# Optimization experiments

Hardware: AMD Instinct MI355X
Metric: run time of the kernel (lower is better)

Reference implementation:

```python
import jax, jax.numpy as jnp
import numpy as np

S, D, H, HD = 3072, 1280, 16, 80
FF = 4 * D
EPS = 1e-6


def layernorm(x, scale, bias):
    mu = jnp.mean(x, axis=-1, keepdims=True)
    var = jnp.mean(jnp.square(x - mu), axis=-1, keepdims=True)
    return (x - mu) * jax.lax.rsqrt(var + EPS) * scale + bias


def rotate_half(x):
    x1 = x[..., : x.shape[-1] // 2]
    x2 = x[..., x.shape[-1] // 2 :]
    return jnp.concatenate([-x2, x1], axis=-1)


def apply_rope(x, freqs):
    # x: (S,H,hd), freqs: (S,hd/2)
    cos = jnp.repeat(jnp.cos(freqs), 2, axis=-1)[:, None, :]  # (S,1,hd)
    sin = jnp.repeat(jnp.sin(freqs), 2, axis=-1)[:, None, :]
    return x * cos + rotate_half(x) * sin


def quick_gelu(x):
    return x * jax.nn.sigmoid(1.702 * x)


def setup_inputs() -> dict:
    key = jax.random.key(0)
    ks = jax.random.split(key, 12)
    s = 0.02
    return {
        "hidden_states": jax.random.normal(ks[0], (S, D), jnp.float32),
        "rotary_pos_emb": jax.random.normal(ks[1], (S, HD // 2), jnp.float32),
        "ln1_scale": jnp.ones((D,), jnp.float32),
        "ln1_bias": jnp.zeros((D,), jnp.float32),
        "ln2_scale": jnp.ones((D,), jnp.float32),
        "ln2_bias": jnp.zeros((D,), jnp.float32),
        "qkv_w": jax.random.normal(ks[2], (D, 3 * D), jnp.float32) * s,
        "qkv_b": jnp.zeros((3 * D,), jnp.float32),
        "proj_w": jax.random.normal(ks[3], (D, D), jnp.float32) * s,
        "proj_b": jnp.zeros((D,), jnp.float32),
        "fc1_w": jax.random.normal(ks[4], (D, FF), jnp.float32) * s,
        "fc1_b": jnp.zeros((FF,), jnp.float32),
        "fc2_w": jax.random.normal(ks[5], (FF, D), jnp.float32) * s,
        "fc2_b": jnp.zeros((D,), jnp.float32),
        "cu_seqlens": jnp.array([0, 1024, 2048, 3072], jnp.int32),
    }


def reference(hidden_states, rotary_pos_emb, ln1_scale, ln1_bias, ln2_scale,
              ln2_bias, qkv_w, qkv_b, proj_w, proj_b, fc1_w, fc1_b, fc2_w,
              fc2_b, cu_seqlens):
    x = hidden_states  # (S, D)
    h = layernorm(x, ln1_scale, ln1_bias)
    qkv = (h @ qkv_w + qkv_b).reshape(S, 3, H, HD)
    q, k, v = qkv[:, 0], qkv[:, 1], qkv[:, 2]  # each (S, H, hd)
    q = apply_rope(q, rotary_pos_emb)
    k = apply_rope(k, rotary_pos_emb)

    # block-diagonal varlen mask from cu_seqlens (same segment attends)
    ids = jnp.arange(S)
    seg = jnp.searchsorted(cu_seqlens, ids, side="right")  # (S,)
    valid = seg[:, None] == seg[None, :]  # (S, S)
    bias = jnp.where(valid, 0.0, jnp.finfo(q.dtype).min)

    scale = 1.0 / jnp.sqrt(jnp.asarray(HD, q.dtype))
    scores = jnp.einsum("qhd,khd->hqk", q, k) * scale + bias
    probs = jax.nn.softmax(scores.astype(jnp.float32), axis=-1).astype(q.dtype)
    attn = jnp.einsum("hqk,khd->qhd", probs, v).reshape(S, D)
    attn = attn @ proj_w + proj_b

    x = x + attn
    h2 = layernorm(x, ln2_scale, ln2_bias)
    mlp = quick_gelu(h2 @ fc1_w + fc1_b) @ fc2_w + fc2_b
    return x + mlp
```

## Files before the change

kernel.cpp:

```cpp
#include <hip/hip_runtime.h>

typedef __bf16 bf16x8 __attribute__((ext_vector_type(8)));
typedef float f32x4 __attribute__((ext_vector_type(4)));
typedef unsigned short u16;
typedef u16 u16x4 __attribute__((ext_vector_type(4)));
typedef u16 u16x8 __attribute__((ext_vector_type(8)));
typedef float float4v __attribute__((ext_vector_type(4)));

__device__ __forceinline__ u16 f2bf(float f) {
    __bf16 b = (__bf16)f;
    return __builtin_bit_cast(unsigned short, b);
}
__device__ __forceinline__ float bf2f(u16 x) {
    __bf16 b = __builtin_bit_cast(__bf16, x);
    return (float)b;
}

__device__ __forceinline__ void gld16(const void* g, void* l) {
    __builtin_amdgcn_global_load_lds((const __attribute__((address_space(1))) void*)g,
                                     (__attribute__((address_space(3))) void*)l, 16, 0, 0);
}

__device__ __forceinline__ int xcd_swz(int orig, int nwg) {
    const int q = nwg >> 3, r = nwg & 7;
    const int xcd = orig & 7, pos = orig >> 3;
    return (xcd < r ? xcd * (q + 1) : r * (q + 1) + (xcd - r) * q) + pos;
}

__global__ __launch_bounds__(256) void transpose_kernel(
    const float* __restrict__ W, u16* __restrict__ WT, int K, int N)
{
    __shared__ u16 tile[64][65];
    const int tx = threadIdx.x & 63, ty = threadIdx.x >> 6;
    const int n0 = blockIdx.x * 64, k0 = blockIdx.y * 64;
    #pragma unroll
    for (int i = ty; i < 64; i += 4)
        tile[i][tx] = f2bf(W[(size_t)(k0 + i) * N + n0 + tx]);
    __syncthreads();
    #pragma unroll
    for (int i = ty; i < 64; i += 4)
        WT[(size_t)(n0 + i) * K + k0 + tx] = tile[tx][i];
}

__global__ __launch_bounds__(256) void ln_kernel(
    const float* __restrict__ x, const float* __restrict__ sc,
    const float* __restrict__ bias, u16* __restrict__ out)
{
    const int row = blockIdx.x, t = threadIdx.x;
    const float* xr = x + (size_t)row * 1280;
    float v[5], s1 = 0.f, s2 = 0.f;
    #pragma unroll
    for (int i = 0; i < 5; i++) {
        v[i] = xr[t + i * 256];
        s1 += v[i];
        s2 += v[i] * v[i];
    }
    #pragma unroll
    for (int off = 32; off; off >>= 1) {
        s1 += __shfl_down(s1, off);
        s2 += __shfl_down(s2, off);
    }
    __shared__ float rA[4], rB[4];
    if ((t & 63) == 0) { rA[t >> 6] = s1; rB[t >> 6] = s2; }
    __syncthreads();
    s1 = rA[0] + rA[1] + rA[2] + rA[3];
    s2 = rB[0] + rB[1] + rB[2] + rB[3];
    const float mu = s1 * (1.f / 1280.f);
    const float var = s2 * (1.f / 1280.f) - mu * mu;
    const float rstd = rsqrtf(var + 1e-6f);
    #pragma unroll
    for (int i = 0; i < 5; i++) {
        const int d = t + i * 256;
        out[(size_t)row * 1280 + d] = f2bf((v[i] - mu) * rstd * sc[d] + bias[d]);
    }
}

template <int GELU, int OUTB, int SPLIT>
__global__ __launch_bounds__(512, 2) void gemm256_kernel(
    const u16* __restrict__ A, const u16* __restrict__ BT,
    const float* __restrict__ bias,
    float* __restrict__ outF, u16* __restrict__ outB,
    int M, int N, int K)
{
    __shared__ u16 As[2][256 * 64];
    __shared__ u16 Bs[2][256 * 64];
    const int tid = threadIdx.x, lane = tid & 63, wave = tid >> 6;
    const int nwg = gridDim.x * gridDim.y;
    const int bid = xcd_swz(blockIdx.y * gridDim.x + blockIdx.x, nwg);
    const int m0 = (bid / gridDim.x) * 256, n0 = (bid % gridDim.x) * 256;
    const int wr = wave >> 2, wc = wave & 3;
    const int wm = wr * 128, wn = wc * 64;
    const int lr = lane & 15, lh = lane >> 4;

    const int kchunk = K / SPLIT;
    const int kz = (SPLIT > 1) ? blockIdx.z : 0;
    const int kbeg = kz * kchunk;
    const int niter = kchunk >> 7;

    const int sr = lane >> 3;
    const int sc8 = (lane & 7) ^ sr;

    f32x4 acc[8][4] = {};
    bf16x8 bq[4][2];

    auto stgA = [&](int t, int h) {
        const int buf = t & 1;
        #pragma unroll
        for (int j = 0; j < 2; j++) {
            const int row = h * 128 + j * 64 + wave * 8 + sr;
            gld16(A + (size_t)(m0 + row) * K + kbeg + t * 64 + sc8 * 8,
                  &As[buf][h * 8192 + j * 4096 + wave * 512]);
        }
    };
    auto stgB = [&](int t, int h) {
        const int buf = t & 1;
        #pragma unroll
        for (int j = 0; j < 2; j++) {
            const int row = h * 128 + j * 64 + wave * 8 + sr;
            gld16(BT + (size_t)(n0 + row) * K + kbeg + t * 64 + sc8 * 8,
                  &Bs[buf][h * 8192 + j * 4096 + wave * 512]);
        }
    };

#define PHASE(BUF, Q, STGSTMT, WAITSTMT)                                        \
    {                                                                           \
        if ((Q) == 0) {                                                         \
            _Pragma("unroll") for (int ni = 0; ni < 4; ni++) {                  \
                const int row = wn + ni * 16 + lr;                              \
                _Pragma("unroll") for (int kk = 0; kk < 2; kk++)                \
                    bq[ni][kk] = *reinterpret_cast<const bf16x8*>(              \
                        &Bs[BUF][row * 64 + ((kk * 4 + lh) ^ (row & 7)) * 8]);  \
            }                                                                   \
        }                                                                       \
        bf16x8 afq[2][2];                                                       \
        _Pragma("unroll") for (int m2 = 0; m2 < 2; m2++) {                      \
            const int row = wm + (Q) * 32 + m2 * 16 + lr;                       \
            _Pragma("unroll") for (int kk = 0; kk < 2; kk++)                    \
                afq[m2][kk] = *reinterpret_cast<const bf16x8*>(                 \
                    &As[BUF][row * 64 + ((kk * 4 + lh) ^ (row & 7)) * 8]);      \
        }                                                                       \
        STGSTMT;                                                                \
        __builtin_amdgcn_s_barrier();                                           \
        asm volatile("s_waitcnt lgkmcnt(0)" ::: "memory");                      \
        __builtin_amdgcn_s_setprio(1);                                          \
        _Pragma("unroll") for (int kk = 0; kk < 2; kk++)                        \
            _Pragma("unroll") for (int m2 = 0; m2 < 2; m2++)                    \
                _Pragma("unroll") for (int ni = 0; ni < 4; ni++)                \
                    acc[(Q) * 2 + m2][ni] =                                     \
                        __builtin_amdgcn_mfma_f32_16x16x32_bf16(                \
                            afq[m2][kk], bq[ni][kk], acc[(Q) * 2 + m2][ni],     \
                            0, 0, 0);                                           \
        __builtin_amdgcn_s_setprio(0);                                          \
        WAITSTMT;                                                               \
        __builtin_amdgcn_s_barrier();                                           \
    }

    stgB(0, 0); stgB(0, 1);
    stgA(0, 0); stgA(0, 1);
    stgB(1, 0); stgB(1, 1);
    asm volatile("s_waitcnt vmcnt(4)" ::: "memory");
    __builtin_amdgcn_s_barrier();

    for (int i = 0; i < niter - 1; i++) {
        const int t0 = 2 * i, t1 = 2 * i + 1;
        PHASE(0, 0, stgA(t1, 0), (void)0);
        PHASE(0, 1, stgA(t1, 1), (void)0);
        PHASE(0, 2, stgB(t0 + 2, 0), (void)0);
        PHASE(0, 3, stgB(t0 + 2, 1),
              asm volatile("s_waitcnt vmcnt(4)" ::: "memory"));
        PHASE(1, 0, stgA(t0 + 2, 0), (void)0);
        PHASE(1, 1, stgA(t0 + 2, 1), (void)0);
        PHASE(1, 2, stgB(t1 + 2, 0), (void)0);
        PHASE(1, 3, stgB(t1 + 2, 1),
              asm volatile("s_waitcnt vmcnt(4)" ::: "memory"));
    }
    {
        const int t1 = 2 * niter - 1;
        PHASE(0, 0, stgA(t1, 0), (void)0);
        PHASE(0, 1, stgA(t1, 1), (void)0);
        PHASE(0, 2, (void)0, (void)0);
        PHASE(0, 3, (void)0,
              asm volatile("s_waitcnt vmcnt(0)" ::: "memory"));
        PHASE(1, 0, (void)0, (void)0);
        PHASE(1, 1, (void)0, (void)0);
        PHASE(1, 2, (void)0, (void)0);
        PHASE(1, 3, (void)0, (void)0);
    }
#undef PHASE

    if (SPLIT > 1) {
        float* pf = outF + (size_t)kz * M * N;
        #pragma unroll
        for (int mi = 0; mi < 8; mi++)
            #pragma unroll
            for (int ni = 0; ni < 4; ni++) {
                const int col = n0 + wn + ni * 16 + lr;
                #pragma unroll
                for (int r = 0; r < 4; r++) {
                    const int rowg = m0 + wm + mi * 16 + lh * 4 + r;
                    pf[(size_t)rowg * N + col] = acc[mi][ni][r];
                }
            }
        return;
    }

    #pragma unroll
    for (int mi = 0; mi < 8; mi++) {
        #pragma unroll
        for (int ni = 0; ni < 4; ni++) {
            const int col = n0 + wn + ni * 16 + lr;
            const float bv = bias[col];
            #pragma unroll
            for (int r = 0; r < 4; r++) {
                const int rowg = m0 + wm + mi * 16 + lh * 4 + r;
                float v = acc[mi][ni][r] + bv;
                if (GELU) v = v * (1.0f / (1.0f + __expf(-1.702f * v)));
                if (OUTB) outB[(size_t)rowg * N + col] = f2bf(v);
            }
        }
    }
}

template <int GELU, int RES, int OUTF, int OUTB, int SPLIT>
__global__ __launch_bounds__(256) void gemm_kernel(
    const u16* __restrict__ A, const u16* __restrict__ BT,
    const float* __restrict__ bias, const float* __restrict__ res,
    float* __restrict__ outF, u16* __restrict__ outB,
    int M, int N, int K)
{
    __shared__ u16 As[128 * 64];
    __shared__ u16 Bs[128 * 64];
    const int tid = threadIdx.x, lane = tid & 63, wave = tid >> 6;
    const int nwg = gridDim.x * gridDim.y;
    const int bid = xcd_swz(blockIdx.y * gridDim.x + blockIdx.x, nwg);
    const int m0 = (bid / gridDim.x) * 128, n0 = (bid % gridDim.x) * 128;
    const int wm = (wave >> 1) * 64, wn = (wave & 1) * 64;
    const int lr = lane & 15, lh = lane >> 4;
    const int srow = lane >> 3;
    const int schunk = (lane & 7) ^ (srow & 7);

    const int kchunk = K / SPLIT;
    const int kz = (SPLIT > 1) ? blockIdx.z : 0;
    const int kbeg = kz * kchunk, kend = kbeg + kchunk;

    f32x4 acc[4][4] = {};

    for (int k0 = kbeg; k0 < kend; k0 += 64) {
        #pragma unroll
        for (int s = 0; s < 4; s++) {
            const int seg = wave + s * 4;
            const int row = seg * 8 + srow;
            gld16(A + (size_t)(m0 + row) * K + k0 + schunk * 8, &As[seg * 512]);
            gld16(BT + (size_t)(n0 + row) * K + k0 + schunk * 8, &Bs[seg * 512]);
        }
        asm volatile("s_waitcnt vmcnt(0)" ::: "memory");
        __syncthreads();

        bf16x8 af[4][2], bfr[4][2];
        #pragma unroll
        for (int mi = 0; mi < 4; mi++) {
            const int row = wm + mi * 16 + lr;
            #pragma unroll
            for (int kk = 0; kk < 2; kk++) {
                const int cb = (kk * 64 + lh * 16) ^ ((row & 7) << 4);
                af[mi][kk] = *reinterpret_cast<const bf16x8*>((const char*)As + row * 128 + cb);
            }
        }
        #pragma unroll
        for (int ni = 0; ni < 4; ni++) {
            const int row = wn + ni * 16 + lr;
            #pragma unroll
            for (int kk = 0; kk < 2; kk++) {
                const int cb = (kk * 64 + lh * 16) ^ ((row & 7) << 4);
                bfr[ni][kk] = *reinterpret_cast<const bf16x8*>((const char*)Bs + row * 128 + cb);
            }
        }
        #pragma unroll
        for (int kk = 0; kk < 2; kk++)
            #pragma unroll
            for (int mi = 0; mi < 4; mi++)
                #pragma unroll
                for (int ni = 0; ni < 4; ni++)
                    acc[mi][ni] = __builtin_amdgcn_mfma_f32_16x16x32_bf16(
                        af[mi][kk], bfr[ni][kk], acc[mi][ni], 0, 0, 0);
        __syncthreads();
    }

    if (SPLIT > 1) {
        float* pf = outF + (size_t)kz * M * N;
        #pragma unroll
        for (int mi = 0; mi < 4; mi++)
            #pragma unroll
            for (int ni = 0; ni < 4; ni++) {
                const int col = n0 + wn + ni * 16 + lr;
                #pragma unroll
                for (int r = 0; r < 4; r++) {
                    const int rowg = m0 + wm + mi * 16 + lh * 4 + r;
                    pf[(size_t)rowg * N + col] = acc[mi][ni][r];
                }
            }
        return;
    }

    #pragma unroll
    for (int mi = 0; mi < 4; mi++) {
        #pragma unroll
        for (int ni = 0; ni < 4; ni++) {
            const int col = n0 + wn + ni * 16 + lr;
            const float bv = bias[col];
            #pragma unroll
            for (int r = 0; r < 4; r++) {
                const int rowg = m0 + wm + mi * 16 + lh * 4 + r;
                float v = acc[mi][ni][r] + bv;
                if (RES) v += res[(size_t)rowg * N + col];
                if (GELU) v = v * (1.0f / (1.0f + __expf(-1.702f * v)));
                if (OUTF) outF[(size_t)rowg * N + col] = v;
                if (OUTB) outB[(size_t)rowg * N + col] = f2bf(v);
            }
        }
    }
}

__global__ __launch_bounds__(256) void reduce4_kernel(
    const float* __restrict__ parts, const float* __restrict__ bias,
    const float* __restrict__ res, float* __restrict__ out, int N, size_t MN)
{
    const size_t i4 = ((size_t)blockIdx.x * 256 + threadIdx.x) * 4;
    if (i4 >= MN) return;
    float4v a = *reinterpret_cast<const float4v*>(parts + i4);
    a += *reinterpret_cast<const float4v*>(parts + MN + i4);
    a += *reinterpret_cast<const float4v*>(parts + 2 * MN + i4);
    a += *reinterpret_cast<const float4v*>(parts + 3 * MN + i4);
    a += *reinterpret_cast<const float4v*>(res + i4);
    const int col = (int)(i4 % N);
    a += *reinterpret_cast<const float4v*>(bias + col);
    *reinterpret_cast<float4v*>(out + i4) = a;
}

__global__ __launch_bounds__(256) void rope_kernel(
    const u16* __restrict__ qkv, const float* __restrict__ freqs,
    u16* __restrict__ qp, u16* __restrict__ kp, u16* __restrict__ vt)
{
    const int s = blockIdx.x, t = threadIdx.x;
    const float scale = 0.1118033988749895f;
    __shared__ float cs[40], sn[40];
    if (t < 40) {
        const float f = freqs[(size_t)s * 40 + t];
        cs[t] = cosf(f);
        sn[t] = sinf(f);
    }
    __syncthreads();
    const u16* row = qkv + (size_t)s * 3840;
    for (int i = t; i < 1280; i += 256) {
        const int h = i / 80, d = i % 80;
        const float c = cs[d >> 1], sv = sn[d >> 1];
        const float q0 = bf2f(row[i]);
        const float q1 = (d < 40) ? -bf2f(row[i + 40]) : bf2f(row[i - 40]);
        qp[((size_t)h * 3072 + s) * 96 + d] = f2bf((q0 * c + q1 * sv) * scale);
        const float k0 = bf2f(row[1280 + i]);
        const float k1 = (d < 40) ? -bf2f(row[1280 + i + 40]) : bf2f(row[1280 + i - 40]);
        kp[((size_t)h * 3072 + s) * 128 + d] = f2bf(k0 * c + k1 * sv);
        vt[((size_t)h * 80 + d) * 3072 + s] = row[2560 + i];
    }
    {
        const int h = t / 16, d = 80 + (t % 16);
        qp[((size_t)h * 3072 + s) * 96 + d] = 0;
    }
    for (int i = t; i < 768; i += 256) {
        const int h = i / 48, d = 80 + (i % 48);
        kp[((size_t)h * 3072 + s) * 128 + d] = 0;
    }
}

__global__ __launch_bounds__(256) void attn_kernel(
    const u16* __restrict__ qp, const u16* __restrict__ kp,
    const u16* __restrict__ vt, u16* __restrict__ attn_out)
{
    const int tid = threadIdx.x, lane = tid & 63, wave = tid >> 6;
    const int w = xcd_swz(blockIdx.x, 768);
    const int qt = w & 15;
    const int h = (w >> 4) & 15;
    const int sq = w >> 8;
    const int lr = lane & 15, lh = lane >> 4;
    const int qrow = sq * 1024 + qt * 64 + wave * 16;

    __shared__ u16 Ks[2][64 * 128];
    __shared__ u16 Vs[2][80 * 64];
    __shared__ u16 P[4][16 * 72];

    bf16x8 aq[3];
    {
        const u16* qb = qp + ((size_t)h * 3072 + qrow + lr) * 96 + lh * 8;
        #pragma unroll
        for (int d0 = 0; d0 < 3; d0++)
            aq[d0] = *reinterpret_cast<const bf16x8*>(qb + d0 * 32);
    }

    float m = -1e30f, l = 0.f;
    f32x4 acc[5] = {};

    const u16* kseg = kp + ((size_t)h * 3072 + sq * 1024) * 128;
    const u16* vseg = vt + (size_t)h * 80 * 3072 + sq * 1024;

    const int krow_l = lane >> 4;
    const int kch    = lane & 15;
    const int vrow_l = lane >> 3;
    const int vch    = lane & 7;

    auto stageK = [&](int t, int buf) {
        #pragma unroll
        for (int s = 0; s < 4; s++) {
            const int seg = wave + s * 4;
            const int row = seg * 4 + krow_l;
            gld16(kseg + (size_t)(t * 64 + row) * 128 + ((kch ^ (row & 7)) * 8),
                  &Ks[buf][seg * 512]);
        }
    };
    auto stageV = [&](int t, int buf) {
        #pragma unroll
        for (int s = 0; s < 3; s++) {
            const int seg = wave + s * 4;
            if (seg < 10) {
                const int row = seg * 8 + vrow_l;
                gld16(vseg + (size_t)row * 3072 + t * 64 + ((vch ^ (row & 7)) * 8),
                      &Vs[buf][seg * 512]);
            }
        }
    };

    stageK(0, 0);
    stageV(0, 0);
    asm volatile("s_waitcnt vmcnt(0)" ::: "memory");
    __syncthreads();

    for (int t = 0; t < 16; t++) {
        const int cur = t & 1;
        if (t < 15) {
            stageK(t + 1, cur ^ 1);
            stageV(t + 1, cur ^ 1);
        }

        f32x4 sc[4] = {};
        #pragma unroll
        for (int c = 0; c < 4; c++) {
            #pragma unroll
            for (int d0 = 0; d0 < 3; d0++) {
                const int row = c * 16 + lr;
                const int rb = row * 256 + (((d0 * 4 + lh) ^ (row & 7)) << 4);
                bf16x8 kf = *reinterpret_cast<const bf16x8*>((const char*)Ks[cur] + rb);
                sc[c] = __builtin_amdgcn_mfma_f32_16x16x32_bf16(kf, aq[d0], sc[c], 0, 0, 0);
            }
        }

        float pmax = sc[0][0];
        #pragma unroll
        for (int c = 0; c < 4; c++)
            #pragma unroll
            for (int r = 0; r < 4; r++)
                pmax = fmaxf(pmax, sc[c][r]);
        pmax = fmaxf(pmax, __shfl_xor(pmax, 16));
        pmax = fmaxf(pmax, __shfl_xor(pmax, 32));

        if (!__all(pmax - m <= 8.0f)) {
            const float mn = fmaxf(m, pmax);
            const float fac = __expf(m - mn);
            m = mn;
            l *= fac;
            #pragma unroll
            for (int df = 0; df < 5; df++)
                #pragma unroll
                for (int r = 0; r < 4; r++)
                    acc[df][r] *= fac;
        }

        float p[4][4], rs = 0.f;
        #pragma unroll
        for (int c = 0; c < 4; c++)
            #pragma unroll
            for (int r = 0; r < 4; r++) {
                p[c][r] = __expf(sc[c][r] - m);
                rs += p[c][r];
            }
        rs += __shfl_xor(rs, 16);
        rs += __shfl_xor(rs, 32);
        l += rs;

        #pragma unroll
        for (int c = 0; c < 4; c++) {
            u16x4 pw;
            #pragma unroll
            for (int r = 0; r < 4; r++)
                pw[r] = f2bf(p[c][r]);
            *reinterpret_cast<u16x4*>((char*)P[wave] + lr * 144 + c * 32 + lh * 8) = pw;
        }
        asm volatile("s_waitcnt lgkmcnt(0)" ::: "memory");

        #pragma unroll
        for (int ks = 0; ks < 2; ks++) {
            bf16x8 pa = *reinterpret_cast<const bf16x8*>(
                (const char*)P[wave] + lr * 144 + ks * 64 + lh * 16);
            #pragma unroll
            for (int df = 0; df < 5; df++) {
                const int row = df * 16 + lr;
                const int vb = row * 128 + (((ks * 4 + lh) ^ (row & 7)) << 4);
                bf16x8 vf = *reinterpret_cast<const bf16x8*>((const char*)Vs[cur] + vb);
                acc[df] = __builtin_amdgcn_mfma_f32_16x16x32_bf16(vf, pa, acc[df], 0, 0, 0);
            }
        }

        asm volatile("s_waitcnt vmcnt(0)" ::: "memory");
        __syncthreads();
    }

    const float invl = 1.0f / l;
    u16* orow = attn_out + (size_t)(qrow + lr) * 1280 + h * 80;
    #pragma unroll
    for (int df = 0; df < 5; df++) {
        u16x4 o;
        #pragma unroll
        for (int r = 0; r < 4; r++)
            o[r] = f2bf(acc[df][r] * invl);
        *reinterpret_cast<u16x4*>(orow + df * 16 + lh * 4) = o;
    }
}

extern "C" void kernel_launch(void* const* d_in, const int* in_sizes, int n_in,
                              void* d_out, int out_size, void* d_ws, size_t ws_size,
                              hipStream_t stream) {
    const float* hidden = (const float*)d_in[0];
    const float* rot    = (const float*)d_in[1];
    const float* ln1s   = (const float*)d_in[2];
    const float* ln1b   = (const float*)d_in[3];
    const float* ln2s   = (const float*)d_in[4];
    const float* ln2b   = (const float*)d_in[5];
    const float* qkvw   = (const float*)d_in[6];
    const float* qkvb   = (const float*)d_in[7];
    const float* projw  = (const float*)d_in[8];
    const float* projb  = (const float*)d_in[9];
    const float* fc1w   = (const float*)d_in[10];
    const float* fc1b   = (const float*)d_in[11];
    const float* fc2w   = (const float*)d_in[12];
    const float* fc2b   = (const float*)d_in[13];
    float* out = (float*)d_out;

    char* p = (char*)d_ws;
    auto alloc = [&](size_t n) { char* r = p; p += (n + 255) & ~(size_t)255; return r; };
    u16* qkvwT  = (u16*)alloc((size_t)3840 * 1280 * 2);
    u16* projwT = (u16*)alloc((size_t)1280 * 1280 * 2);
    u16* fc1wT  = (u16*)alloc((size_t)5120 * 1280 * 2);
    u16* fc2wT  = (u16*)alloc((size_t)1280 * 5120 * 2);
    u16* hbuf   = (u16*)alloc((size_t)3072 * 1280 * 2);
    u16* qkvbf  = (u16*)alloc((size_t)3072 * 5120 * 2);
    u16* attnb  = (u16*)alloc((size_t)3072 * 1280 * 2);
    float* xmid = (float*)alloc((size_t)3072 * 1280 * 4);
    float* parts = (float*)alloc((size_t)4 * 3072 * 1280 * 4);
    u16* qp2 = (u16*)parts;
    u16* kp2 = qp2 + (size_t)16 * 3072 * 96;
    u16* vt2 = kp2 + (size_t)16 * 3072 * 128;
    u16* h2   = hbuf;
    u16* mlp1 = qkvbf;
    const size_t MN = (size_t)3072 * 1280;

    transpose_kernel<<<dim3(3840 / 64, 1280 / 64), 256, 0, stream>>>(qkvw, qkvwT, 1280, 3840);
    transpose_kernel<<<dim3(1280 / 64, 1280 / 64), 256, 0, stream>>>(projw, projwT, 1280, 1280);
    transpose_kernel<<<dim3(5120 / 64, 1280 / 64), 256, 0, stream>>>(fc1w, fc1wT, 1280, 5120);
    transpose_kernel<<<dim3(1280 / 64, 5120 / 64), 256, 0, stream>>>(fc2w, fc2wT, 5120, 1280);

    ln_kernel<<<3072, 256, 0, stream>>>(hidden, ln1s, ln1b, hbuf);
    gemm256_kernel<0, 1, 1><<<dim3(15, 12), 512, 0, stream>>>(
        hbuf, qkvwT, qkvb, nullptr, qkvbf, 3072, 3840, 1280);
    rope_kernel<<<3072, 256, 0, stream>>>(qkvbf, rot, qp2, kp2, vt2);
    attn_kernel<<<768, 256, 0, stream>>>(qp2, kp2, vt2, attnb);
    gemm_kernel<0, 0, 1, 0, 4><<<dim3(10, 24, 4), 256, 0, stream>>>(
        attnb, projwT, projb, nullptr, parts, nullptr, 3072, 1280, 1280);
    reduce4_kernel<<<(int)(MN / 4 / 256), 256, 0, stream>>>(parts, projb, hidden, xmid, 1280, MN);
    ln_kernel<<<3072, 256, 0, stream>>>(xmid, ln2s, ln2b, h2);
    gemm256_kernel<1, 1, 1><<<dim3(20, 12), 512, 0, stream>>>(
        h2, fc1wT, fc1b, nullptr, mlp1, 3072, 5120, 1280);
    gemm256_kernel<0, 0, 4><<<dim3(5, 12, 4), 512, 0, stream>>>(
        mlp1, fc2wT, fc2b, parts, nullptr, 3072, 1280, 5120);
    reduce4_kernel<<<(int)(MN / 4 / 256), 256, 0, stream>>>(parts, fc2b, xmid, out, 1280, MN);
}
```

Before: 318.2 us.

## Merge weight transposes, fuse reduce with LayerNorm2, reuse K smem for P

The four weight-transpose launches become one kernel that picks the matrix from the block index. The split-K reduction for the projection is fused with the second LayerNorm, so xmid is not re-read from global memory and one launch is removed. In attention, the per-wave P buffer is dropped and probabilities are written into the unused padding columns (96-127) of the current K tile in two halves, which lowers LDS use and may raise occupancy. The cost is an extra LDS wait and serialized PV halves.

New measurement: 289.5 us. 1.1x faster.

```diff
diff --git a/kernel.cpp b/kernel.cpp
--- a/kernel.cpp
+++ b/kernel.cpp
@@ -27,12 +27,21 @@
     return (xcd < r ? xcd * (q + 1) : r * (q + 1) + (xcd - r) * q) + pos;
 }
 
-__global__ __launch_bounds__(256) void transpose_kernel(
-    const float* __restrict__ W, u16* __restrict__ WT, int K, int N)
+__global__ __launch_bounds__(256) void transpose_all_kernel(
+    const float* __restrict__ qkvw, const float* __restrict__ projw,
+    const float* __restrict__ fc1w, const float* __restrict__ fc2w,
+    u16* __restrict__ qkvwT, u16* __restrict__ projwT,
+    u16* __restrict__ fc1wT, u16* __restrict__ fc2wT)
 {
     __shared__ u16 tile[64][65];
+    int bid = blockIdx.x;
+    const float* W; u16* WT; int K, N, nx;
+    if (bid < 1200)      { W = qkvw;  WT = qkvwT;  K = 1280; N = 3840; nx = 60; }
+    else if (bid < 1600) { bid -= 1200; W = projw; WT = projwT; K = 1280; N = 1280; nx = 20; }
+    else if (bid < 3200) { bid -= 1600; W = fc1w;  WT = fc1wT;  K = 1280; N = 5120; nx = 80; }
+    else                 { bid -= 3200; W = fc2w;  WT = fc2wT;  K = 5120; N = 1280; nx = 20; }
     const int tx = threadIdx.x & 63, ty = threadIdx.x >> 6;
-    const int n0 = blockIdx.x * 64, k0 = blockIdx.y * 64;
+    const int n0 = (bid % nx) * 64, k0 = (bid / nx) * 64;
     #pragma unroll
     for (int i = ty; i < 64; i += 4)
         tile[i][tx] = f2bf(W[(size_t)(k0 + i) * N + n0 + tx]);
@@ -72,6 +81,45 @@
     for (int i = 0; i < 5; i++) {
         const int d = t + i * 256;
         out[(size_t)row * 1280 + d] = f2bf((v[i] - mu) * rstd * sc[d] + bias[d]);
+    }
+}
+
+__global__ __launch_bounds__(256) void reduce4_ln_kernel(
+    const float* __restrict__ parts, const float* __restrict__ bias,
+    const float* __restrict__ res, const float* __restrict__ lns,
+    const float* __restrict__ lnb, float* __restrict__ xmid,
+    u16* __restrict__ h2, size_t MN)
+{
+    const int row = blockIdx.x, t = threadIdx.x;
+    float v[5], s1 = 0.f, s2 = 0.f;
+    #pragma unroll
+    for (int i = 0; i < 5; i++) {
+        const int d = t + i * 256;
+        const size_t idx = (size_t)row * 1280 + d;
+        float a = parts[idx] + parts[MN + idx] + parts[2 * MN + idx] + parts[3 * MN + idx]
+                + res[idx] + bias[d];
+        v[i] = a;
+        xmid[idx] = a;
+        s1 += a;
+        s2 += a * a;
+    }
+    #pragma unroll
+    for (int off = 32; off; off >>= 1) {
+        s1 += __shfl_down(s1, off);
+        s2 += __shfl_down(s2, off);
+    }
+    __shared__ float rA[4], rB[4];
+    if ((t & 63) == 0) { rA[t >> 6] = s1; rB[t >> 6] = s2; }
+    __syncthreads();
+    s1 = rA[0] + rA[1] + rA[2] + rA[3];
+    s2 = rB[0] + rB[1] + rB[2] + rB[3];
+    const float mu = s1 * (1.f / 1280.f);
+    const float var = s2 * (1.f / 1280.f) - mu * mu;
+    const float rstd = rsqrtf(var + 1e-6f);
+    #pragma unroll
+    for (int i = 0; i < 5; i++) {
+        const int d = t + i * 256;
+        h2[(size_t)row * 1280 + d] = f2bf((v[i] - mu) * rstd * lns[d] + lnb[d]);
     }
 }
 
@@ -386,7 +434,6 @@
 
     __shared__ u16 Ks[2][64 * 128];
     __shared__ u16 Vs[2][80 * 64];
-    __shared__ u16 P[4][16 * 72];
 
     bf16x8 aq[3];
     {
@@ -433,6 +480,9 @@
     asm volatile("s_waitcnt vmcnt(0)" ::: "memory");
     __syncthreads();
 
+    const int prow = wave * 16 + lr;
+    const int psw = prow & 7;
+
     for (int t = 0; t < 16; t++) {
         const int cur = t & 1;
         if (t < 15) {
@@ -485,24 +535,46 @@
         rs += __shfl_xor(rs, 32);
         l += rs;
 
-        #pragma unroll
-        for (int c = 0; c < 4; c++) {
+        char* pb = (char*)Ks[cur] + prow * 256;
+        const int prd = ((12 + lh) ^ psw) << 4;
+
+        #pragma unroll
+        for (int cc = 0; cc < 2; cc++) {
             u16x4 pw;
             #pragma unroll
             for (int r = 0; r < 4; r++)
-                pw[r] = f2bf(p[c][r]);
-            *reinterpret_cast<u16x4*>((char*)P[wave] + lr * 144 + c * 32 + lh * 8) = pw;
+                pw[r] = f2bf(p[cc][r]);
+            *reinterpret_cast<u16x4*>(
+                pb + (((12 + cc * 2 + (lh >> 1)) ^ psw) << 4) + (lh & 1) * 8) = pw;
         }
         asm volatile("s_waitcnt lgkmcnt(0)" ::: "memory");
-
-        #pragma unroll
-        for (int ks = 0; ks < 2; ks++) {
-            bf16x8 pa = *reinterpret_cast<const bf16x8*>(
-                (const char*)P[wave] + lr * 144 + ks * 64 + lh * 16);
+        {
+            bf16x8 pa = *reinterpret_cast<const bf16x8*>(pb + prd);
+            asm volatile("s_waitcnt lgkmcnt(0)" ::: "memory");
             #pragma unroll
             for (int df = 0; df < 5; df++) {
                 const int row = df * 16 + lr;
-                const int vb = row * 128 + (((ks * 4 + lh) ^ (row & 7)) << 4);
+                const int vb = row * 128 + ((lh ^ (row & 7)) << 4);
+                bf16x8 vf = *reinterpret_cast<const bf16x8*>((const char*)Vs[cur] + vb);
+                acc[df] = __builtin_amdgcn_mfma_f32_16x16x32_bf16(vf, pa, acc[df], 0, 0, 0);
+            }
+        }
+        #pragma unroll
+        for (int cc = 0; cc < 2; cc++) {
+            u16x4 pw;
+            #pragma unroll
+            for (int r = 0; r < 4; r++)
+                pw[r] = f2bf(p[2 + cc][r]);
+            *reinterpret_cast<u16x4*>(
+                pb + (((12 + cc * 2 + (lh >> 1)) ^ psw) << 4) + (lh & 1) * 8) = pw;
+        }
+        asm volatile("s_waitcnt lgkmcnt(0)" ::: "memory");
+        {
+            bf16x8 pa = *reinterpret_cast<const bf16x8*>(pb + prd);
+            #pragma unroll
+            for (int df = 0; df < 5; df++) {
+                const int row = df * 16 + lr;
+                const int vb = row * 128 + (((4 + lh) ^ (row & 7)) << 4);
                 bf16x8 vf = *reinterpret_cast<const bf16x8*>((const char*)Vs[cur] + vb);
                 acc[df] = __builtin_amdgcn_mfma_f32_16x16x32_bf16(vf, pa, acc[df], 0, 0, 0);
             }
@@ -561,10 +633,8 @@
     u16* mlp1 = qkvbf;
     const size_t MN = (size_t)3072 * 1280;
 
-    transpose_kernel<<<dim3(3840 / 64, 1280 / 64), 256, 0, stream>>>(qkvw, qkvwT, 1280, 3840);
-    transpose_kernel<<<dim3(1280 / 64, 1280 / 64), 256, 0, stream>>>(projw, projwT, 1280, 1280);
-    transpose_kernel<<<dim3(5120 / 64, 1280 / 64), 256, 0, stream>>>(fc1w, fc1wT, 1280, 5120);
-    transpose_kernel<<<dim3(1280 / 64, 5120 / 64), 256, 0, stream>>>(fc2w, fc2wT, 5120, 1280);
+    transpose_all_kernel<<<4800, 256, 0, stream>>>(
+        qkvw, projw, fc1w, fc2w, qkvwT, projwT, fc1wT, fc2wT);
 
     ln_kernel<<<3072, 256, 0, stream>>>(hidden, ln1s, ln1b, hbuf);
     gemm256_kernel<0, 1, 1><<<dim3(15, 12), 512, 0, stream>>>(
@@ -573,8 +643,8 @@
     attn_kernel<<<768, 256, 0, stream>>>(qp2, kp2, vt2, attnb);
     gemm_kernel<0, 0, 1, 0, 4><<<dim3(10, 24, 4), 256, 0, stream>>>(
         attnb, projwT, projb, nullptr, parts, nullptr, 3072, 1280, 1280);
-    reduce4_kernel<<<(int)(MN / 4 / 256), 256, 0, stream>>>(parts, projb, hidden, xmid, 1280, MN);
-    ln_kernel<<<3072, 256, 0, stream>>>(xmid, ln2s, ln2b, h2);
+    reduce4_ln_kernel<<<3072, 256, 0, stream>>>(
+        parts, projb, hidden, ln2s, ln2b, xmid, h2, MN);
     gemm256_kernel<1, 1, 1><<<dim3(20, 12), 512, 0, stream>>>(
         h2, fc1wT, fc1b, nullptr, mlp1, 3072, 5120, 1280);
     gemm256_kernel<0, 0, 4><<<dim3(5, 12, 4), 512, 0, stream>>>(
```
